# Optimization experiments

Measured on AMD Instinct MI355X. Metric: run time of the kernel, lower is better.

## Reference

```python
import jax, jax.numpy as jnp
import numpy as np

INV_SQRT2 = 0.7071067811865476
SCALES = 3


def dwt_analysis(x, dec_lo, dec_hi, scales):
    """Multi-level 1D DWT along last axis (pywt/ptwt convention).
    x: [B, D]. dec_lo/dec_hi are cross-correlation filters (torch conv1d
    semantics, i.e. the flipped pywt decomposition filters as stored by the
    repo). Returns [cA_s | cD_s | ... | cD_1] truncated to the last D columns
    (identity for Haar on power-of-two D)."""
    flen = dec_lo.shape[0]
    pad = (2 * flen - 3) // 2  # ptwt zero-pad; 0 for Haar (flen=2)
    filt = jnp.stack([dec_lo, dec_hi])[:, None, :]  # [2, 1, flen]
    lo = x[:, None, :]  # [B, 1, D]
    highs = []
    for _ in range(scales):
        out = jax.lax.conv_general_dilated(
            lo, filt, window_strides=(2,), padding=[(pad, pad)],
            dimension_numbers=('NCH', 'OIH', 'NCH'))  # [B, 2, D/2]
        lo = out[:, 0:1, :]
        highs.append(out[:, 1, :])
    coeffs = jnp.concatenate([lo[:, 0, :]] + highs[::-1], axis=-1)
    return coeffs[:, -x.shape[-1]:]


def setup_inputs() -> dict:
    key = jax.random.key(0)
    k1, k2, k3, k4, k5 = jax.random.split(key, 5)
    B, D = 4096, 4096
    x = jax.random.normal(k1, (B, D), jnp.float32)
    diag_s = jax.random.normal(k2, (D,), jnp.float32)
    diag_g = jax.random.normal(k3, (D,), jnp.float32)
    diag_b = jax.random.normal(k4, (D,), jnp.float32)
    perm = jax.random.permutation(k5, jnp.arange(D))  # random column permutation
    # Haar analysis filters in cross-correlation (torch conv1d) orientation
    dec_lo = jnp.array([INV_SQRT2, INV_SQRT2], jnp.float32)
    dec_hi = jnp.array([INV_SQRT2, -INV_SQRT2], jnp.float32)
    return {"x": x, "diag_s": diag_s, "diag_g": diag_g, "diag_b": diag_b,
            "dec_lo": dec_lo, "dec_hi": dec_hi, "perm": perm, "scales": SCALES}


def reference(x, diag_s, diag_g, diag_b, dec_lo, dec_hi, perm, scales):
    # mul_b: x @ diag(b) == columnwise scale (same math, no O(d^2) matmul)
    h = x * diag_b
    h = dwt_analysis(h, dec_lo, dec_hi, scales)
    # mul_p: x @ P for a permutation matrix == column gather
    h = jnp.take(h, perm, axis=1)
    h = h * diag_g  # mul_g
    h = dwt_analysis(h, dec_lo, dec_hi, scales)
    return h * diag_s  # mul_s
```

## Files before the change

### kernel.cpp

```cpp
#include <hip/hip_runtime.h>


#define D   4096
#define NT  256
#define VPT (D / NT)

static __device__ __forceinline__ constexpr float inv_sqrt2() {
    return 0.70710678118654752440f;
}

__global__ __launch_bounds__(NT) void wavelet_row_kernel(
    const float* __restrict__ x,
    const float* __restrict__ diag_s,
    const float* __restrict__ diag_g,
    const float* __restrict__ diag_b,
    const int*   __restrict__ perm,
    float*       __restrict__ out)
{
    __shared__ float buf[D];

    const int tid = threadIdx.x;
    const size_t row = blockIdx.x;
    const float* xr = x + row * (size_t)D;
    float* orow = out + row * (size_t)D;

    {
        const float4* x4 = (const float4*)xr;
        const float4* b4 = (const float4*)diag_b;
        float4* s4 = (float4*)buf;
        for (int i = tid; i < D / 4; i += NT) {
            float4 v = x4[i];
            float4 b = b4[i];
            v.x *= b.x; v.y *= b.y; v.z *= b.z; v.w *= b.w;
            s4[i] = v;
        }
    }
    __syncthreads();

    #pragma unroll
    for (int lvl = 0; lvl < 3; ++lvl) {
        const int len  = D >> lvl;
        const int half = len >> 1;
        float a[VPT / 2], b[VPT / 2];
        int cnt = 0;
        for (int p = tid; p < half; p += NT) {
            a[cnt] = buf[2 * p];
            b[cnt] = buf[2 * p + 1];
            ++cnt;
        }
        __syncthreads();
        cnt = 0;
        for (int p = tid; p < half; p += NT) {
            buf[p]        = (a[cnt] + b[cnt]) * inv_sqrt2();
            buf[half + p] = (a[cnt] - b[cnt]) * inv_sqrt2();
            ++cnt;
        }
        __syncthreads();
    }

    {
        int   pj[VPT];
        float gv[VPT];
        #pragma unroll
        for (int k = 0; k < VPT; ++k) {
            const int j = tid + k * NT;
            pj[k] = perm[j];
        }
        #pragma unroll
        for (int k = 0; k < VPT; ++k) {
            const int j = tid + k * NT;
            gv[k] = buf[pj[k]] * diag_g[j];
        }
        __syncthreads();
        #pragma unroll
        for (int k = 0; k < VPT; ++k) {
            buf[tid + k * NT] = gv[k];
        }
        __syncthreads();
    }

    #pragma unroll
    for (int lvl = 0; lvl < 3; ++lvl) {
        const int len  = D >> lvl;
        const int half = len >> 1;
        float a[VPT / 2], b[VPT / 2];
        int cnt = 0;
        for (int p = tid; p < half; p += NT) {
            a[cnt] = buf[2 * p];
            b[cnt] = buf[2 * p + 1];
            ++cnt;
        }
        __syncthreads();
        cnt = 0;
        for (int p = tid; p < half; p += NT) {
            buf[p]        = (a[cnt] + b[cnt]) * inv_sqrt2();
            buf[half + p] = (a[cnt] - b[cnt]) * inv_sqrt2();
            ++cnt;
        }
        __syncthreads();
    }

    {
        const float4* s4 = (const float4*)buf;
        const float4* d4 = (const float4*)diag_s;
        float4* o4 = (float4*)orow;
        for (int i = tid; i < D / 4; i += NT) {
            float4 v = s4[i];
            float4 s = d4[i];
            v.x *= s.x; v.y *= s.y; v.z *= s.z; v.w *= s.w;
            o4[i] = v;
        }
    }
}

extern "C" void kernel_launch(void* const* d_in, const int* in_sizes, int n_in,
                              void* d_out, int out_size, void* d_ws, size_t ws_size,
                              hipStream_t stream) {
    const float* x      = (const float*)d_in[0];
    const float* diag_s = (const float*)d_in[1];
    const float* diag_g = (const float*)d_in[2];
    const float* diag_b = (const float*)d_in[3];
    const int* perm     = (const int*)d_in[6];
    float* out          = (float*)d_out;

    const int B = 4096;
    wavelet_row_kernel<<<B, NT, 0, stream>>>(x, diag_s, diag_g, diag_b, perm, out);
}
```

Baseline: 138.2 us.

## Compute 3-level Haar DWT in registers per thread, use shared memory only for permutation

```diff
diff --git a/kernel.cpp b/kernel.cpp
--- a/kernel.cpp
+++ b/kernel.cpp
@@ -3,10 +3,33 @@
 
 #define D   4096
 #define NT  256
-#define VPT (D / NT)
 
-static __device__ __forceinline__ constexpr float inv_sqrt2() {
-    return 0.70710678118654752440f;
+#define C_INV_SQRT2 0.70710678118654752440f
+
+static __device__ __forceinline__ int swz(int i) {
+    return i ^ ((i >> 5) & 31);
+}
+
+static __device__ __forceinline__ void dwt3_reg(const float v[16],
+                                                float a3[2], float d3[2],
+                                                float d2[4], float d1[8]) {
+    float a1[8];
+    #pragma unroll
+    for (int j = 0; j < 8; ++j) {
+        a1[j] = (v[2 * j] + v[2 * j + 1]) * C_INV_SQRT2;
+        d1[j] = (v[2 * j] - v[2 * j + 1]) * C_INV_SQRT2;
+    }
+    float a2[4];
+    #pragma unroll
+    for (int j = 0; j < 4; ++j) {
+        a2[j] = (a1[2 * j] + a1[2 * j + 1]) * C_INV_SQRT2;
+        d2[j] = (a1[2 * j] - a1[2 * j + 1]) * C_INV_SQRT2;
+    }
+    #pragma unroll
+    for (int j = 0; j < 2; ++j) {
+        a3[j] = (a2[2 * j] + a2[2 * j + 1]) * C_INV_SQRT2;
+        d3[j] = (a2[2 * j] - a2[2 * j + 1]) * C_INV_SQRT2;
+    }
 }
 
 __global__ __launch_bounds__(NT) void wavelet_row_kernel(
@@ -19,96 +42,91 @@
 {
     __shared__ float buf[D];
 
-    const int tid = threadIdx.x;
+    const int t = threadIdx.x;
     const size_t row = blockIdx.x;
-    const float* xr = x + row * (size_t)D;
-    float* orow = out + row * (size_t)D;
 
+    float v[16];
     {
-        const float4* x4 = (const float4*)xr;
+        const float4* x4 = (const float4*)(x + row * (size_t)D);
         const float4* b4 = (const float4*)diag_b;
-        float4* s4 = (float4*)buf;
-        for (int i = tid; i < D / 4; i += NT) {
-            float4 v = x4[i];
-            float4 b = b4[i];
-            v.x *= b.x; v.y *= b.y; v.z *= b.z; v.w *= b.w;
-            s4[i] = v;
+        #pragma unroll
+        for (int k = 0; k < 4; ++k) {
+            float4 xv = x4[4 * t + k];
+            float4 bv = b4[4 * t + k];
+            v[4 * k + 0] = xv.x * bv.x;
+            v[4 * k + 1] = xv.y * bv.y;
+            v[4 * k + 2] = xv.z * bv.z;
+            v[4 * k + 3] = xv.w * bv.w;
         }
     }
+
+    float a3[2], d3[2], d2[4], d1[8];
+    dwt3_reg(v, a3, d3, d2, d1);
+
+    #pragma unroll
+    for (int j = 0; j < 2; ++j) buf[swz(2 * t + j)]        = a3[j];
+    #pragma unroll
+    for (int j = 0; j < 2; ++j) buf[swz(512 + 2 * t + j)]  = d3[j];
+    #pragma unroll
+    for (int j = 0; j < 4; ++j) buf[swz(1024 + 4 * t + j)] = d2[j];
+    #pragma unroll
+    for (int j = 0; j < 8; ++j) buf[swz(2048 + 8 * t + j)] = d1[j];
+
     __syncthreads();
 
-    #pragma unroll
-    for (int lvl = 0; lvl < 3; ++lvl) {
-        const int len  = D >> lvl;
-        const int half = len >> 1;
-        float a[VPT / 2], b[VPT / 2];
-        int cnt = 0;
-        for (int p = tid; p < half; p += NT) {
-            a[cnt] = buf[2 * p];
-            b[cnt] = buf[2 * p + 1];
-            ++cnt;
+    float w[16];
+    {
+        const int4*   p4 = (const int4*)perm;
+        const float4* g4 = (const float4*)diag_g;
+        int pidx[16];
+        #pragma unroll
+        for (int k = 0; k < 4; ++k) {
+            int4 pv = p4[4 * t + k];
+            pidx[4 * k + 0] = pv.x;
+            pidx[4 * k + 1] = pv.y;
+            pidx[4 * k + 2] = pv.z;
+            pidx[4 * k + 3] = pv.w;
         }
-        __syncthreads();
-        cnt = 0;
-        for (int p = tid; p < half; p += NT) {
-            buf[p]        = (a[cnt] + b[cnt]) * inv_sqrt2();
-            buf[half + p] = (a[cnt] - b[cnt]) * inv_sqrt2();
-            ++cnt;
+        #pragma unroll
+        for (int k = 0; k < 4; ++k) {
+            float4 gv = g4[4 * t + k];
+            w[4 * k + 0] = buf[swz(pidx[4 * k + 0])] * gv.x;
+            w[4 * k + 1] = buf[swz(pidx[4 * k + 1])] * gv.y;
+            w[4 * k + 2] = buf[swz(pidx[4 * k + 2])] * gv.z;
+            w[4 * k + 3] = buf[swz(pidx[4 * k + 3])] * gv.w;
         }
-        __syncthreads();
     }
 
+    float b3[2], e3[2], e2[4], e1[8];
+    dwt3_reg(w, b3, e3, e2, e1);
+
+    float* orow = out + row * (size_t)D;
     {
-        int   pj[VPT];
-        float gv[VPT];
+        const float2* s2 = (const float2*)diag_s;
+        float2* o2 = (float2*)orow;
+        float2 sv, ov;
+        sv = s2[t];
+        ov.x = b3[0] * sv.x; ov.y = b3[1] * sv.y;
+        o2[t] = ov;
+        sv = s2[256 + t];
+        ov.x = e3[0] * sv.x; ov.y = e3[1] * sv.y;
+        o2[256 + t] = ov;
+    }
+    {
+        const float4* s4 = (const float4*)diag_s;
+        float4* o4 = (float4*)orow;
+        float4 sv = s4[256 + t];
+        float4 ov;
+        ov.x = e2[0] * sv.x; ov.y = e2[1] * sv.y;
+        ov.z = e2[2] * sv.z; ov.w = e2[3] * sv.w;
+        o4[256 + t] = ov;
         #pragma unroll
-        for (int k = 0; k < VPT; ++k) {
-            const int j = tid + k * NT;
-            pj[k] = perm[j];
-        }
-        #pragma unroll
-        for (int k = 0; k < VPT; ++k) {
-            const int j = tid + k * NT;
-            gv[k] = buf[pj[k]] * diag_g[j];
-        }
-        __syncthreads();
-        #pragma unroll
-        for (int k = 0; k < VPT; ++k) {
-            buf[tid + k * NT] = gv[k];
-        }
-        __syncthreads();
-    }
-
-    #pragma unroll
-    for (int lvl = 0; lvl < 3; ++lvl) {
-        const int len  = D >> lvl;
-        const int half = len >> 1;
-        float a[VPT / 2], b[VPT / 2];
-        int cnt = 0;
-        for (int p = tid; p < half; p += NT) {
-            a[cnt] = buf[2 * p];
-            b[cnt] = buf[2 * p + 1];
-            ++cnt;
-        }
-        __syncthreads();
-        cnt = 0;
-        for (int p = tid; p < half; p += NT) {
-            buf[p]        = (a[cnt] + b[cnt]) * inv_sqrt2();
-            buf[half + p] = (a[cnt] - b[cnt]) * inv_sqrt2();
-            ++cnt;
-        }
-        __syncthreads();
-    }
-
-    {
-        const float4* s4 = (const float4*)buf;
-        const float4* d4 = (const float4*)diag_s;
-        float4* o4 = (float4*)orow;
-        for (int i = tid; i < D / 4; i += NT) {
-            float4 v = s4[i];
-            float4 s = d4[i];
-            v.x *= s.x; v.y *= s.y; v.z *= s.z; v.w *= s.w;
-            o4[i] = v;
+        for (int k = 0; k < 2; ++k) {
+            float4 sw = s4[512 + 2 * t + k];
+            float4 ow;
+            ow.x = e1[4 * k + 0] * sw.x; ow.y = e1[4 * k + 1] * sw.y;
+            ow.z = e1[4 * k + 2] * sw.z; ow.w = e1[4 * k + 3] * sw.w;
+            o4[512 + 2 * t + k] = ow;
         }
     }
 }
```

New measurement: 139.9 us. About the same (+1.3%).
